# Kernel optimization log

Hardware: AMD Instinct MI355X
Metric: run time of the kernel (lower is better)

Reference implementation:

```python
import jax, jax.numpy as jnp
import numpy as np

N_NODES = 50000
N_EDGES = 600000
N_GRAPHS = 500


def gcn_conv(x, src, dst, W, b, n_nodes):
    # PyG GCNConv: add self-loops, symmetric normalization D^-1/2 (A+I) D^-1/2, then XW + b
    h = x @ W  # [N, F_out]
    loop = jnp.arange(n_nodes)
    s = jnp.concatenate([src, loop])
    d = jnp.concatenate([dst, loop])
    deg = jax.ops.segment_sum(jnp.ones_like(d, dtype=h.dtype), d, num_segments=n_nodes)
    dinv = jnp.where(deg > 0, jax.lax.rsqrt(jnp.maximum(deg, 1.0)), 0.0)
    norm = dinv[s] * dinv[d]  # [E+N]
    msg = h[s] * norm[:, None]  # gather + scale
    out = jax.ops.segment_sum(msg, d, num_segments=n_nodes)  # scatter-add
    return out + b


def setup_inputs() -> dict:
    key = jax.random.key(0)
    ks = jax.random.split(key, 12)
    F_in, H, Hf, D_out = 128, 128, 64, 1
    x = jax.random.normal(ks[0], (N_NODES, F_in), dtype=jnp.float32)
    edge_index = jax.random.randint(ks[1], (2, N_EDGES), 0, N_NODES, dtype=jnp.int64)
    batch = jnp.sort(jax.random.randint(ks[2], (N_NODES,), 0, N_GRAPHS, dtype=jnp.int64))
    def glorot(k, shape):
        lim = np.sqrt(6.0 / (shape[0] + shape[1]))
        return jax.random.uniform(k, shape, jnp.float32, -lim, lim)
    return {
        "x": x, "edge_index": edge_index, "batch": batch,
        "W1": glorot(ks[3], (F_in, H)), "b1": jnp.zeros((H,), jnp.float32),
        "W2": glorot(ks[4], (H, H)), "b2": jnp.zeros((H,), jnp.float32),
        "W3": glorot(ks[5], (H, H)), "b3": jnp.zeros((H,), jnp.float32),
        "Wf1": glorot(ks[6], (H, Hf)), "bf1": jnp.zeros((Hf,), jnp.float32),
        "Wf2": glorot(ks[7], (Hf, D_out)), "bf2": jnp.zeros((D_out,), jnp.float32),
    }


def reference(x, edge_index, batch, W1, b1, W2, b2, W3, b3, Wf1, bf1, Wf2, bf2):
    src, dst = edge_index[0], edge_index[1]
    n = x.shape[0]
    h = jax.nn.relu(gcn_conv(x, src, dst, W1, b1, n))
    h = jax.nn.relu(gcn_conv(h, src, dst, W2, b2, n))
    h = jax.nn.relu(gcn_conv(h, src, dst, W3, b3, n))
    # global_mean_pool: segment mean over graphs
    sums = jax.ops.segment_sum(h, batch, num_segments=N_GRAPHS)
    cnts = jax.ops.segment_sum(jnp.ones((n,), h.dtype), batch, num_segments=N_GRAPHS)
    hg = sums / jnp.maximum(cnts, 1.0)[:, None]  # [G, 128]
    h = jax.nn.relu(hg @ Wf1 + bf1)
    return h @ Wf2 + bf2
```

## Files before the change

### kernel.cpp

```cpp
#include <hip/hip_runtime.h>

#define N_NODES 50000
#define N_EDGES 600000
#define N_GRAPHS 500
#define F 128

typedef short bf16x8 __attribute__((ext_vector_type(8)));
typedef float f32x4 __attribute__((ext_vector_type(4)));
union U4H8 { uint4 u; bf16x8 h; };

__device__ inline unsigned pk_bf16(float a, float b) {
    unsigned ua = __float_as_uint(a), ub = __float_as_uint(b);
    ua = (ua + 0x7fffu + ((ua >> 16) & 1u)) >> 16;
    ub = (ub + 0x7fffu + ((ub >> 16) & 1u)) >> 16;
    return ua | (ub << 16);
}
__device__ inline float bf16_rnd(float x) {
    unsigned u = __float_as_uint(x);
    u = (u + 0x7fffu + ((u >> 16) & 1u)) & 0xffff0000u;
    return __uint_as_float(u);
}
__device__ inline unsigned short bf16_1(float a) {
    unsigned ua = __float_as_uint(a);
    return (unsigned short)((ua + 0x7fffu + ((ua >> 16) & 1u)) >> 16);
}
#define BF_LO(u) __uint_as_float((u) << 16)
#define BF_HI(u) __uint_as_float((u) & 0xffff0000u)

#define G_CVT  3125
#define G_HIST 2344
#define G_PREPW 24
#define G_BND  196

__global__ __launch_bounds__(256) void k_prep(const float* __restrict__ x, unsigned short* __restrict__ xb,
                                              const int* __restrict__ dst, int* __restrict__ cnt,
                                              const float* __restrict__ W1, const float* __restrict__ W2,
                                              const float* __restrict__ W3,
                                              uint4* __restrict__ Whi, uint4* __restrict__ Wlo,
                                              const int* __restrict__ batch, int* __restrict__ gs) {
    int b = blockIdx.x, tid = threadIdx.x;
    if (b < G_CVT) {
        int idx = b * 256 + tid;
        if (idx < N_NODES * F / 8) {
            const float4* xr = (const float4*)(x + (size_t)idx * 8);
            float4 a = xr[0], c = xr[1];
            uint4 o;
            o.x = pk_bf16(a.x, a.y); o.y = pk_bf16(a.z, a.w);
            o.z = pk_bf16(c.x, c.y); o.w = pk_bf16(c.z, c.w);
            ((uint4*)xb)[idx] = o;
        }
    } else if (b < G_CVT + G_HIST) {
        int e = (b - G_CVT) * 256 + tid;
        if (e < N_EDGES) atomicAdd(&cnt[dst[e]], 1);
    } else if (b < G_CVT + G_HIST + G_PREPW) {
        int idx = (b - G_CVT - G_HIST) * 256 + tid;
        int layer = idx >> 11;
        const float* W = (layer == 0) ? W1 : (layer == 1) ? W2 : W3;
        int t = idx & 2047;
        int lane = t & 63, sc = t >> 6;
        int s = sc >> 3, c = sc & 7;
        int q = lane >> 4, m = lane & 15;
        int k0 = 32 * s + 8 * q, n0 = 16 * c + m;
        float w[8], h[8];
        #pragma unroll
        for (int j = 0; j < 8; ++j) {
            w[j] = W[(k0 + j) * F + n0];
            h[j] = bf16_rnd(w[j]);
        }
        uint4 uh, ul;
        uh.x = pk_bf16(h[0], h[1]); uh.y = pk_bf16(h[2], h[3]);
        uh.z = pk_bf16(h[4], h[5]); uh.w = pk_bf16(h[6], h[7]);
        ul.x = pk_bf16(w[0] - h[0], w[1] - h[1]); ul.y = pk_bf16(w[2] - h[2], w[3] - h[3]);
        ul.z = pk_bf16(w[4] - h[4], w[5] - h[5]); ul.w = pk_bf16(w[6] - h[6], w[7] - h[7]);
        Whi[idx] = uh;
        Wlo[idx] = ul;
    } else {
        int i = (b - G_CVT - G_HIST - G_PREPW) * 256 + tid;
        if (i < N_NODES) {
            int bi = batch[i];
            if (i == 0) {
                for (int g = 0; g <= bi; ++g) gs[g] = 0;
            } else {
                int bp = batch[i - 1];
                for (int g = bp + 1; g <= bi; ++g) gs[g] = i;
            }
            if (i == N_NODES - 1) {
                for (int g = bi + 1; g <= N_GRAPHS; ++g) gs[g] = N_NODES;
            }
        }
    }
}

__global__ __launch_bounds__(256) void k_scan1(const int* __restrict__ cnt, int* __restrict__ row_ptr,
                                               int* __restrict__ blksums, float* __restrict__ dinv, int n) {
    __shared__ int s[256];
    int i = blockIdx.x * 256 + threadIdx.x;
    int v = (i < n) ? cnt[i] : 0;
    if (i < n) dinv[i] = rsqrtf((float)(v + 1));
    s[threadIdx.x] = v;
    __syncthreads();
    for (int off = 1; off < 256; off <<= 1) {
        int t = (threadIdx.x >= off) ? s[threadIdx.x - off] : 0;
        __syncthreads();
        s[threadIdx.x] += t;
        __syncthreads();
    }
    if (i < n) row_ptr[i] = s[threadIdx.x] - v;
    if (threadIdx.x == 255) blksums[blockIdx.x] = s[255];
}

__global__ __launch_bounds__(256) void k_scan23(int* __restrict__ row_ptr, const int* __restrict__ blksums,
                                                int n, int ne) {
    __shared__ int s[256];
    int tid = threadIdx.x;
    s[tid] = (tid < (int)blockIdx.x) ? blksums[tid] : 0;
    __syncthreads();
    for (int off = 128; off > 0; off >>= 1) {
        if (tid < off) s[tid] += s[tid + off];
        __syncthreads();
    }
    int base = s[0];
    int i = blockIdx.x * 256 + tid;
    if (i < n) row_ptr[i] += base;
    if (i == 0) row_ptr[n] = ne;
}

__global__ __launch_bounds__(256) void k_fill(const int* __restrict__ src, const int* __restrict__ dst,
                                              const int* __restrict__ row_ptr, int* __restrict__ cnt,
                                              const float* __restrict__ dinv,
                                              int2* __restrict__ esw, int ne) {
    int e = blockIdx.x * 256 + threadIdx.x;
    if (e < ne) {
        int d = dst[e];
        int s = src[e];
        int pos = row_ptr[d] + atomicSub(&cnt[d], 1) - 1;
        esw[pos] = make_int2(s, __float_as_int(dinv[s]));
    }
}

#define TN 16
#define GP2 136
#define MAXE_L 512
__global__ __launch_bounds__(256) void k_fused(const int* __restrict__ row_ptr,
                                               const int2* __restrict__ esw,
                                               const float* __restrict__ dinv,
                                               const unsigned short* __restrict__ Hin,
                                               const uint4* __restrict__ Whi,
                                               const uint4* __restrict__ Wlo,
                                               const float* __restrict__ bias,
                                               unsigned short* __restrict__ Hout, int n) {
    __shared__ unsigned short Gb[TN * GP2];
    __shared__ uint2 eL[MAXE_L];
    __shared__ int rp[TN + 1];
    __shared__ float ddl[TN];
    int tid = threadIdx.x;
    int d0 = blockIdx.x * TN;

    int dTN = d0 + TN; if (dTN > n) dTN = n;
    int e0 = row_ptr[d0];
    int e1 = row_ptr[dTN];
    if (tid <= TN) {
        int d = d0 + tid; if (d > n) d = n;
        rp[tid] = row_ptr[d];
    }
    if (tid < TN) {
        int d = d0 + tid;
        ddl[tid] = (d < n) ? dinv[d] : 0.f;
    }
    int nE = e1 - e0; if (nE > MAXE_L) nE = MAXE_L;
    for (int i = tid; i < nE; i += 256) eL[i] = ((const uint2*)esw)[e0 + i];
    __syncthreads();

    int grp = tid >> 4, sub = tid & 15;

    {
        int nl = grp;
        int node = d0 + nl;
        float4 accL = make_float4(0.f, 0.f, 0.f, 0.f);
        float4 accH = make_float4(0.f, 0.f, 0.f, 0.f);
        if (node < n) {
            int beg = rp[nl], end = rp[nl + 1];
            float dd = ddl[nl];
            uint4 srow = ((const uint4*)(Hin + (size_t)node * F))[sub];
            float ws = dd * dd;
            accL.x = BF_LO(srow.x) * ws;
            accL.y = BF_HI(srow.x) * ws;
            accL.z = BF_LO(srow.y) * ws;
            accL.w = BF_HI(srow.y) * ws;
            accH.x = BF_LO(srow.z) * ws;
            accH.y = BF_HI(srow.z) * ws;
            accH.z = BF_LO(srow.w) * ws;
            accH.w = BF_HI(srow.w) * ws;
            for (int c = beg; c < end; c += 8) {
                int sjs[8];
                #pragma unroll
                for (int j = 0; j < 8; ++j) {
                    int e = c + j;
                    int sj = node;
                    if (e < end) {
                        int off = e - e0;
                        sj = (off < MAXE_L) ? (int)((const unsigned*)eL)[2 * off]
                                            : ((const uint2*)esw)[e].x;
                    }
                    sjs[j] = sj;
                }
                uint4 rows[8];
                #pragma unroll
                for (int j = 0; j < 8; ++j)
                    rows[j] = ((const uint4*)(Hin + (size_t)sjs[j] * F))[sub];
                #pragma unroll
                for (int j = 0; j < 8; ++j) {
                    int e = c + j;
                    float wj = 0.f;
                    if (e < end) {
                        int off = e - e0;
                        unsigned wb = (off < MAXE_L) ? ((const unsigned*)eL)[2 * off + 1]
                                                     : (unsigned)((const uint2*)esw)[e].y;
                        wj = __uint_as_float(wb) * dd;
                    }
                    accL.x = fmaf(BF_LO(rows[j].x), wj, accL.x);
                    accL.y = fmaf(BF_HI(rows[j].x), wj, accL.y);
                    accL.z = fmaf(BF_LO(rows[j].y), wj, accL.z);
                    accL.w = fmaf(BF_HI(rows[j].y), wj, accL.w);
                    accH.x = fmaf(BF_LO(rows[j].z), wj, accH.x);
                    accH.y = fmaf(BF_HI(rows[j].z), wj, accH.y);
                    accH.z = fmaf(BF_LO(rows[j].w), wj, accH.z);
                    accH.w = fmaf(BF_HI(rows[j].w), wj, accH.w);
                }
            }
        }
        uint4 o;
        o.x = pk_bf16(accL.x, accL.y);
        o.y = pk_bf16(accL.z, accL.w);
        o.z = pk_bf16(accH.x, accH.y);
        o.w = pk_bf16(accH.z, accH.w);
        *(uint4*)&Gb[nl * GP2 + 8 * sub] = o;
    }
    __syncthreads();

    int wave = tid >> 6, lane = tid & 63;
    int q = lane >> 4, m = lane & 15;
    f32x4 acc[2];
    acc[0] = (f32x4){0.f, 0.f, 0.f, 0.f};
    acc[1] = (f32x4){0.f, 0.f, 0.f, 0.f};
    #pragma unroll
    for (int s = 0; s < 4; ++s) {
        U4H8 a;
        a.u = *(const uint4*)&Gb[m * GP2 + 32 * s + 8 * q];
        #pragma unroll
        for (int cc = 0; cc < 2; ++cc) {
            int c = wave * 2 + cc;
            U4H8 bh, bl;
            bh.u = Whi[(s * 8 + c) * 64 + lane];
            bl.u = Wlo[(s * 8 + c) * 64 + lane];
            acc[cc] = __builtin_amdgcn_mfma_f32_16x16x32_bf16(a.h, bh.h, acc[cc], 0, 0, 0);
            acc[cc] = __builtin_amdgcn_mfma_f32_16x16x32_bf16(a.h, bl.h, acc[cc], 0, 0, 0);
        }
    }
    __syncthreads();

    #pragma unroll
    for (int cc = 0; cc < 2; ++cc) {
        int c = wave * 2 + cc;
        float bb = bias[16 * c + m];
        #pragma unroll
        for (int r = 0; r < 4; ++r)
            Gb[(4 * q + r) * GP2 + 16 * c + m] = bf16_1(fmaxf(acc[cc][r] + bb, 0.f));
    }
    __syncthreads();
    {
        int row = tid >> 4, c8 = tid & 15;
        int node = d0 + row;
        if (node < n) {
            uint4 o = *(const uint4*)&Gb[row * GP2 + c8 * 8];
            ((uint4*)(Hout + (size_t)node * F))[c8] = o;
        }
    }
}

__global__ __launch_bounds__(256) void k_pool_fc(const unsigned short* __restrict__ Hb,
                                                 const int* __restrict__ gs,
                                                 const float* __restrict__ Wf1,
                                                 const float* __restrict__ bf1,
                                                 const float* __restrict__ Wf2,
                                                 const float* __restrict__ bf2,
                                                 float* __restrict__ out) {
    int g = blockIdx.x;
    int tid = threadIdx.x;
    int start = gs[g], end = gs[g + 1];

    __shared__ float hs[4][F];
    __shared__ float hg[F];
    int wv = tid >> 6, lane = tid & 63;
    int half = lane >> 5, sub = lane & 31;
    float4 a = make_float4(0.f, 0.f, 0.f, 0.f);
    for (int i = start + wv * 2 + half; i < end; i += 8) {
        uint2 v = ((const uint2*)(Hb + (size_t)i * F))[sub];
        a.x += BF_LO(v.x); a.y += BF_HI(v.x);
        a.z += BF_LO(v.y); a.w += BF_HI(v.y);
    }
    a.x += __shfl_xor(a.x, 32, 64);
    a.y += __shfl_xor(a.y, 32, 64);
    a.z += __shfl_xor(a.z, 32, 64);
    a.w += __shfl_xor(a.w, 32, 64);
    if (half == 0) ((float4*)hs[wv])[sub] = a;
    __syncthreads();
    if (tid < F) {
        float inv = 1.0f / (float)((end - start) > 0 ? (end - start) : 1);
        hg[tid] = (hs[0][tid] + hs[1][tid] + hs[2][tid] + hs[3][tid]) * inv;
    }
    __syncthreads();
    if (tid < 64) {
        float acc = bf1[tid];
        #pragma unroll 4
        for (int f = 0; f < F; ++f) acc = fmaf(hg[f], Wf1[f * 64 + tid], acc);
        float v = fmaxf(acc, 0.f) * Wf2[tid];
        #pragma unroll
        for (int off = 32; off > 0; off >>= 1) v += __shfl_down(v, off, 64);
        if (tid == 0) out[g] = v + bf2[0];
    }
}

extern "C" void kernel_launch(void* const* d_in, const int* in_sizes, int n_in,
                              void* d_out, int out_size, void* d_ws, size_t ws_size,
                              hipStream_t stream) {
    const float* x    = (const float*)d_in[0];
    const int* eidx   = (const int*)d_in[1];
    const int* batch  = (const int*)d_in[2];
    const float* W1   = (const float*)d_in[3];
    const float* b1   = (const float*)d_in[4];
    const float* W2   = (const float*)d_in[5];
    const float* b2   = (const float*)d_in[6];
    const float* W3   = (const float*)d_in[7];
    const float* b3   = (const float*)d_in[8];
    const float* Wf1  = (const float*)d_in[9];
    const float* bf1  = (const float*)d_in[10];
    const float* Wf2  = (const float*)d_in[11];
    const float* bf2  = (const float*)d_in[12];
    float* out = (float*)d_out;

    const int* src = eidx;
    const int* dst = eidx + N_EDGES;

    char* p = (char*)d_ws;
    unsigned short* Xb  = (unsigned short*)p;  p += (size_t)N_NODES * F * 2;
    unsigned short* H1  = (unsigned short*)p;  p += (size_t)N_NODES * F * 2;
    unsigned short* H2  = (unsigned short*)p;  p += (size_t)N_NODES * F * 2;
    unsigned short* H3  = (unsigned short*)p;  p += (size_t)N_NODES * F * 2;
    int2* esw   = (int2*)p;    p += (size_t)N_EDGES * sizeof(int2);
    uint4* Whi  = (uint4*)p;   p += (size_t)3 * 2048 * sizeof(uint4);
    uint4* Wlo  = (uint4*)p;   p += (size_t)3 * 2048 * sizeof(uint4);
    float* dinv = (float*)p;   p += (size_t)N_NODES * sizeof(float);
    int* cnt     = (int*)p;    p += (size_t)N_NODES * sizeof(int);
    int* row_ptr = (int*)p;    p += (size_t)(N_NODES + 1) * sizeof(int);
    int* blksums = (int*)p;    p += 256 * sizeof(int);
    int* gs      = (int*)p;    p += (size_t)(N_GRAPHS + 1) * sizeof(int);

    dim3 b256(256);
    int gNodes = (N_NODES + 255) / 256;
    int gEdges = (N_EDGES + 255) / 256;
    int gFused = (N_NODES + TN - 1) / TN;

    hipMemsetAsync(cnt, 0, (size_t)N_NODES * sizeof(int), stream);
    k_prep<<<G_CVT + G_HIST + G_PREPW + G_BND, b256, 0, stream>>>(x, Xb, dst, cnt, W1, W2, W3,
                                                                  Whi, Wlo, batch, gs);

    k_scan1<<<gNodes, b256, 0, stream>>>(cnt, row_ptr, blksums, dinv, N_NODES);
    k_scan23<<<gNodes, b256, 0, stream>>>(row_ptr, blksums, N_NODES, N_EDGES);
    k_fill<<<gEdges, b256, 0, stream>>>(src, dst, row_ptr, cnt, dinv, esw, N_EDGES);

    k_fused<<<gFused, b256, 0, stream>>>(row_ptr, esw, dinv, Xb, Whi,        Wlo,        b1, H1, N_NODES);
    k_fused<<<gFused, b256, 0, stream>>>(row_ptr, esw, dinv, H1, Whi + 2048, Wlo + 2048, b2, H2, N_NODES);
    k_fused<<<gFused, b256, 0, stream>>>(row_ptr, esw, dinv, H2, Whi + 4096, Wlo + 4096, b3, H3, N_NODES);

    k_pool_fc<<<N_GRAPHS, b256, 0, stream>>>(H3, gs, Wf1, bf1, Wf2, bf2, out);
}
```

Baseline: 268.0 us.

## Sort nodes by degree so each fused block aggregates balanced-degree nodes

Builds a degree histogram in the scan kernel, prefix-sums it, and scatters node ids into a degree-bucketed permutation alongside the CSR fill. The fused aggregate+GEMM kernel then processes 16 nodes from the permutation, so nodes with similar in-degree share a block. This is meant to cut the load imbalance where 16-lane groups wait on the highest-degree node. The cost is extra atomics, a perm array, scattered output rows and a non-contiguous esw range per block, which loses the contiguous per-block edge staging.

```diff
diff --git a/kernel.cpp b/kernel.cpp
--- a/kernel.cpp
+++ b/kernel.cpp
@@ -92,25 +92,33 @@
 }
 
 __global__ __launch_bounds__(256) void k_scan1(const int* __restrict__ cnt, int* __restrict__ row_ptr,
-                                               int* __restrict__ blksums, float* __restrict__ dinv, int n) {
+                                               int* __restrict__ blksums, float* __restrict__ dinv,
+                                               int* __restrict__ dh, int n) {
     __shared__ int s[256];
-    int i = blockIdx.x * 256 + threadIdx.x;
+    __shared__ int dhl[64];
+    int tid = threadIdx.x;
+    int i = blockIdx.x * 256 + tid;
+    if (tid < 64) dhl[tid] = 0;
     int v = (i < n) ? cnt[i] : 0;
     if (i < n) dinv[i] = rsqrtf((float)(v + 1));
-    s[threadIdx.x] = v;
-    __syncthreads();
+    s[tid] = v;
+    __syncthreads();
+    if (i < n) atomicAdd(&dhl[v < 63 ? v : 63], 1);
     for (int off = 1; off < 256; off <<= 1) {
-        int t = (threadIdx.x >= off) ? s[threadIdx.x - off] : 0;
+        int t = (tid >= off) ? s[tid - off] : 0;
         __syncthreads();
-        s[threadIdx.x] += t;
+        s[tid] += t;
         __syncthreads();
     }
-    if (i < n) row_ptr[i] = s[threadIdx.x] - v;
-    if (threadIdx.x == 255) blksums[blockIdx.x] = s[255];
+    if (i < n) row_ptr[i] = s[tid] - v;
+    if (tid == 255) blksums[blockIdx.x] = s[255];
+    __syncthreads();
+    if (tid < 64 && dhl[tid] > 0) atomicAdd(&dh[tid], dhl[tid]);
 }
 
 __global__ __launch_bounds__(256) void k_scan23(int* __restrict__ row_ptr, const int* __restrict__ blksums,
-                                                int n, int ne) {
+                                                const int* __restrict__ dh, int* __restrict__ dhoff,
+                                                int* __restrict__ dcur, int n, int ne) {
     __shared__ int s[256];
     int tid = threadIdx.x;
     s[tid] = (tid < (int)blockIdx.x) ? blksums[tid] : 0;
@@ -123,118 +131,143 @@
     int i = blockIdx.x * 256 + tid;
     if (i < n) row_ptr[i] += base;
     if (i == 0) row_ptr[n] = ne;
-}
-
+    if (blockIdx.x == 0 && tid < 64) {
+        int v = dh[tid];
+        int x = v;
+        #pragma unroll
+        for (int off = 1; off < 64; off <<= 1) {
+            int t = __shfl_up(x, off, 64);
+            if (tid >= off) x += t;
+        }
+        dhoff[tid] = x - v;
+        dcur[tid] = 0;
+    }
+}
+
+#define G_FILL 2344
+#define G_PLACE 196
 __global__ __launch_bounds__(256) void k_fill(const int* __restrict__ src, const int* __restrict__ dst,
                                               const int* __restrict__ row_ptr, int* __restrict__ cnt,
                                               const float* __restrict__ dinv,
-                                              int2* __restrict__ esw, int ne) {
-    int e = blockIdx.x * 256 + threadIdx.x;
-    if (e < ne) {
-        int d = dst[e];
-        int s = src[e];
-        int pos = row_ptr[d] + atomicSub(&cnt[d], 1) - 1;
-        esw[pos] = make_int2(s, __float_as_int(dinv[s]));
+                                              int2* __restrict__ esw,
+                                              const int* __restrict__ dhoff, int* __restrict__ dcur,
+                                              int* __restrict__ perm, int ne) {
+    int b = blockIdx.x, tid = threadIdx.x;
+    if (b < G_FILL) {
+        int e = b * 256 + tid;
+        if (e < ne) {
+            int d = dst[e];
+            int s = src[e];
+            int pos = row_ptr[d] + atomicSub(&cnt[d], 1) - 1;
+            esw[pos] = make_int2(s, __float_as_int(dinv[s]));
+        }
+    } else {
+        int i = (b - G_FILL) * 256 + tid;
+        if (i < N_NODES) {
+            int deg = row_ptr[i + 1] - row_ptr[i];
+            if (deg > 63) deg = 63;
+            int slot = dhoff[deg] + atomicAdd(&dcur[deg], 1);
+            perm[slot] = i;
+        }
     }
 }
 
 #define TN 16
 #define GP2 136
-#define MAXE_L 512
+#define CAPG 64
 __global__ __launch_bounds__(256) void k_fused(const int* __restrict__ row_ptr,
                                                const int2* __restrict__ esw,
                                                const float* __restrict__ dinv,
+                                               const int* __restrict__ perm,
                                                const unsigned short* __restrict__ Hin,
                                                const uint4* __restrict__ Whi,
                                                const uint4* __restrict__ Wlo,
                                                const float* __restrict__ bias,
                                                unsigned short* __restrict__ Hout, int n) {
     __shared__ unsigned short Gb[TN * GP2];
-    __shared__ uint2 eL[MAXE_L];
-    __shared__ int rp[TN + 1];
+    __shared__ uint2 eLg[TN][CAPG];
+    __shared__ int nodeL[TN], begL[TN], endL[TN];
     __shared__ float ddl[TN];
     int tid = threadIdx.x;
     int d0 = blockIdx.x * TN;
-
-    int dTN = d0 + TN; if (dTN > n) dTN = n;
-    int e0 = row_ptr[d0];
-    int e1 = row_ptr[dTN];
-    if (tid <= TN) {
-        int d = d0 + tid; if (d > n) d = n;
-        rp[tid] = row_ptr[d];
-    }
+    int grp = tid >> 4, sub = tid & 15;
+
     if (tid < TN) {
-        int d = d0 + tid;
-        ddl[tid] = (d < n) ? dinv[d] : 0.f;
-    }
-    int nE = e1 - e0; if (nE > MAXE_L) nE = MAXE_L;
-    for (int i = tid; i < nE; i += 256) eL[i] = ((const uint2*)esw)[e0 + i];
-    __syncthreads();
-
-    int grp = tid >> 4, sub = tid & 15;
-
+        int slot = d0 + tid;
+        int node = (slot < n) ? perm[slot] : -1;
+        nodeL[tid] = node;
+        if (node >= 0) {
+            begL[tid] = row_ptr[node];
+            endL[tid] = row_ptr[node + 1];
+            ddl[tid] = dinv[node];
+        } else {
+            begL[tid] = 0; endL[tid] = 0; ddl[tid] = 0.f;
+        }
+    }
+    __syncthreads();
+
+    int node = nodeL[grp];
+    int beg = begL[grp], end = endL[grp];
+    int deg = end - beg;
+    float dd = ddl[grp];
+
+    int degc = deg < CAPG ? deg : CAPG;
+    for (int i = sub; i < degc; i += 16) eLg[grp][i] = ((const uint2*)esw)[beg + i];
+
+    float4 accL = make_float4(0.f, 0.f, 0.f, 0.f);
+    float4 accH = make_float4(0.f, 0.f, 0.f, 0.f);
+    if (node >= 0) {
+        uint4 srow = ((const uint4*)(Hin + (size_t)node * F))[sub];
+        float ws = dd * dd;
+        accL.x = BF_LO(srow.x) * ws;
+        accL.y = BF_HI(srow.x) * ws;
+        accL.z = BF_LO(srow.y) * ws;
+        accL.w = BF_HI(srow.y) * ws;
+        accH.x = BF_LO(srow.z) * ws;
+        accH.y = BF_HI(srow.z) * ws;
+        accH.z = BF_LO(srow.w) * ws;
+        accH.w = BF_HI(srow.w) * ws;
+        for (int c = 0; c < deg; c += 8) {
+            int sjs[8];
+            #pragma unroll
+            for (int j = 0; j < 8; ++j) {
+                int e = c + j;
+                int sj = node;
+                if (e < deg) sj = (e < CAPG) ? (int)eLg[grp][e].x
+                                             : ((const uint2*)esw)[beg + e].x;
+                sjs[j] = sj;
+            }
+            uint4 rows[8];
+            #pragma unroll
+            for (int j = 0; j < 8; ++j)
+                rows[j] = ((const uint4*)(Hin + (size_t)sjs[j] * F))[sub];
+            #pragma unroll
+            for (int j = 0; j < 8; ++j) {
+                int e = c + j;
+                float wj = 0.f;
+                if (e < deg) {
+                    unsigned wb = (e < CAPG) ? eLg[grp][e].y
+                                             : (unsigned)((const uint2*)esw)[beg + e].y;
+                    wj = __uint_as_float(wb) * dd;
+                }
+                accL.x = fmaf(BF_LO(rows[j].x), wj, accL.x);
+                accL.y = fmaf(BF_HI(rows[j].x), wj, accL.y);
+                accL.z = fmaf(BF_LO(rows[j].y), wj, accL.z);
+                accL.w = fmaf(BF_HI(rows[j].y), wj, accL.w);
+                accH.x = fmaf(BF_LO(rows[j].z), wj, accH.x);
+                accH.y = fmaf(BF_HI(rows[j].z), wj, accH.y);
+                accH.z = fmaf(BF_LO(rows[j].w), wj, accH.z);
+                accH.w = fmaf(BF_HI(rows[j].w), wj, accH.w);
+            }
+        }
+    }
     {
-        int nl = grp;
-        int node = d0 + nl;
-        float4 accL = make_float4(0.f, 0.f, 0.f, 0.f);
-        float4 accH = make_float4(0.f, 0.f, 0.f, 0.f);
-        if (node < n) {
-            int beg = rp[nl], end = rp[nl + 1];
-            float dd = ddl[nl];
-            uint4 srow = ((const uint4*)(Hin + (size_t)node * F))[sub];
-            float ws = dd * dd;
-            accL.x = BF_LO(srow.x) * ws;
-            accL.y = BF_HI(srow.x) * ws;
-            accL.z = BF_LO(srow.y) * ws;
-            accL.w = BF_HI(srow.y) * ws;
-            accH.x = BF_LO(srow.z) * ws;
-            accH.y = BF_HI(srow.z) * ws;
-            accH.z = BF_LO(srow.w) * ws;
-            accH.w = BF_HI(srow.w) * ws;
-            for (int c = beg; c < end; c += 8) {
-                int sjs[8];
-                #pragma unroll
-                for (int j = 0; j < 8; ++j) {
-                    int e = c + j;
-                    int sj = node;
-                    if (e < end) {
-                        int off = e - e0;
-                        sj = (off < MAXE_L) ? (int)((const unsigned*)eL)[2 * off]
-                                            : ((const uint2*)esw)[e].x;
-                    }
-                    sjs[j] = sj;
-                }
-                uint4 rows[8];
-                #pragma unroll
-                for (int j = 0; j < 8; ++j)
-                    rows[j] = ((const uint4*)(Hin + (size_t)sjs[j] * F))[sub];
-                #pragma unroll
-                for (int j = 0; j < 8; ++j) {
-                    int e = c + j;
-                    float wj = 0.f;
-                    if (e < end) {
-                        int off = e - e0;
-                        unsigned wb = (off < MAXE_L) ? ((const unsigned*)eL)[2 * off + 1]
-                                                     : (unsigned)((const uint2*)esw)[e].y;
-                        wj = __uint_as_float(wb) * dd;
-                    }
-                    accL.x = fmaf(BF_LO(rows[j].x), wj, accL.x);
-                    accL.y = fmaf(BF_HI(rows[j].x), wj, accL.y);
-                    accL.z = fmaf(BF_LO(rows[j].y), wj, accL.z);
-                    accL.w = fmaf(BF_HI(rows[j].y), wj, accL.w);
-                    accH.x = fmaf(BF_LO(rows[j].z), wj, accH.x);
-                    accH.y = fmaf(BF_HI(rows[j].z), wj, accH.y);
-                    accH.z = fmaf(BF_LO(rows[j].w), wj, accH.z);
-                    accH.w = fmaf(BF_HI(rows[j].w), wj, accH.w);
-                }
-            }
-        }
         uint4 o;
         o.x = pk_bf16(accL.x, accL.y);
         o.y = pk_bf16(accL.z, accL.w);
         o.z = pk_bf16(accH.x, accH.y);
         o.w = pk_bf16(accH.z, accH.w);
-        *(uint4*)&Gb[nl * GP2 + 8 * sub] = o;
+        *(uint4*)&Gb[grp * GP2 + 8 * sub] = o;
     }
     __syncthreads();
 
@@ -270,10 +303,10 @@
     __syncthreads();
     {
         int row = tid >> 4, c8 = tid & 15;
-        int node = d0 + row;
-        if (node < n) {
+        int onode = nodeL[row];
+        if (onode >= 0) {
             uint4 o = *(const uint4*)&Gb[row * GP2 + c8 * 8];
-            ((uint4*)(Hout + (size_t)node * F))[c8] = o;
+            ((uint4*)(Hout + (size_t)onode * F))[c8] = o;
         }
     }
 }
@@ -352,26 +385,30 @@
     uint4* Wlo  = (uint4*)p;   p += (size_t)3 * 2048 * sizeof(uint4);
     float* dinv = (float*)p;   p += (size_t)N_NODES * sizeof(float);
     int* cnt     = (int*)p;    p += (size_t)N_NODES * sizeof(int);
+    int* dh      = (int*)p;    p += 64 * sizeof(int);
     int* row_ptr = (int*)p;    p += (size_t)(N_NODES + 1) * sizeof(int);
     int* blksums = (int*)p;    p += 256 * sizeof(int);
     int* gs      = (int*)p;    p += (size_t)(N_GRAPHS + 1) * sizeof(int);
+    int* dhoff   = (int*)p;    p += 64 * sizeof(int);
+    int* dcur    = (int*)p;    p += 64 * sizeof(int);
+    int* perm    = (int*)p;    p += (size_t)N_NODES * sizeof(int);
 
     dim3 b256(256);
     int gNodes = (N_NODES + 255) / 256;
-    int gEdges = (N_EDGES + 255) / 256;
     int gFused = (N_NODES + TN - 1) / TN;
 
-    hipMemsetAsync(cnt, 0, (size_t)N_NODES * sizeof(int), stream);
+    hipMemsetAsync(cnt, 0, ((size_t)N_NODES + 64) * sizeof(int), stream);
     k_prep<<<G_CVT + G_HIST + G_PREPW + G_BND, b256, 0, stream>>>(x, Xb, dst, cnt, W1, W2, W3,
                                                                   Whi, Wlo, batch, gs);
 
-    k_scan1<<<gNodes, b256, 0, stream>>>(cnt, row_ptr, blksums, dinv, N_NODES);
-    k_scan23<<<gNodes, b256, 0, stream>>>(row_ptr, blksums, N_NODES, N_EDGES);
-    k_fill<<<gEdges, b256, 0, stream>>>(src, dst, row_ptr, cnt, dinv, esw, N_EDGES);
-
-    k_fused<<<gFused, b256, 0, stream>>>(row_ptr, esw, dinv, Xb, Whi,        Wlo,        b1, H1, N_NODES);
-    k_fused<<<gFused, b256, 0, stream>>>(row_ptr, esw, dinv, H1, Whi + 2048, Wlo + 2048, b2, H2, N_NODES);
-    k_fused<<<gFused, b256, 0, stream>>>(row_ptr, esw, dinv, H2, Whi + 4096, Wlo + 4096, b3, H3, N_NODES);
+    k_scan1<<<gNodes, b256, 0, stream>>>(cnt, row_ptr, blksums, dinv, dh, N_NODES);
+    k_scan23<<<gNodes, b256, 0, stream>>>(row_ptr, blksums, dh, dhoff, dcur, N_NODES, N_EDGES);
+    k_fill<<<G_FILL + G_PLACE, b256, 0, stream>>>(src, dst, row_ptr, cnt, dinv, esw,
+                                                  dhoff, dcur, perm, N_EDGES);
+
+    k_fused<<<gFused, b256, 0, stream>>>(row_ptr, esw, dinv, perm, Xb, Whi,        Wlo,        b1, H1, N_NODES);
+    k_fused<<<gFused, b256, 0, stream>>>(row_ptr, esw, dinv, perm, H1, Whi + 2048, Wlo + 2048, b2, H2, N_NODES);
+    k_fused<<<gFused, b256, 0, stream>>>(row_ptr, esw, dinv, perm, H2, Whi + 4096, Wlo + 4096, b3, H3, N_NODES);
 
     k_pool_fc<<<N_GRAPHS, b256, 0, stream>>>(H3, gs, Wf1, bf1, Wf2, bf2, out);
 }
```

Measured after the change: 414.2 us. 54.5% more time.
